# Kernel tuning notes

Measured on AMD Instinct MI355X. Metric: run time of the kernel, lower is better.

The kernel has to match this reference:

```python
import jax, jax.numpy as jnp
import numpy as np

N_NODES = 50000
N_EDGES = 800000
N_FEAT = 256


def setup_inputs() -> dict:
    key = jax.random.key(0)
    k_h, k_src, k_dst, k_w1, k_w2 = jax.random.split(key, 5)
    h = jax.random.normal(k_h, (N_NODES, N_FEAT), dtype=jnp.float32)
    src = jax.random.randint(k_src, (N_EDGES,), 0, N_NODES, dtype=jnp.int32)
    dst = jax.random.randint(k_dst, (N_EDGES,), 0, N_NODES, dtype=jnp.int32)
    # Kaiming-uniform-ish init like nn.Linear defaults
    b1 = 1.0 / np.sqrt(2 * N_FEAT)
    b2 = 1.0 / np.sqrt(N_FEAT)
    W1_w = jax.random.uniform(k_w1, (N_FEAT, 2 * N_FEAT), dtype=jnp.float32, minval=-b1, maxval=b1)
    W1_b = jnp.zeros((N_FEAT,), dtype=jnp.float32)
    W2_w = jax.random.uniform(k_w2, (1, N_FEAT), dtype=jnp.float32, minval=-b2, maxval=b2)
    W2_b = jnp.zeros((1,), dtype=jnp.float32)
    return {"h": h, "src": src, "dst": dst, "W1_w": W1_w, "W1_b": W1_b, "W2_w": W2_w, "W2_b": W2_b}


def reference(h, src, dst, W1_w, W1_b, W2_w, W2_b):
    # Gather per-edge endpoint features and concat along feature dim: [E, 2F]
    e = jnp.concatenate([h[src], h[dst]], axis=-1)
    # 2-layer MLP: Linear -> ReLU -> Linear, squeeze to per-edge score [E]
    hid = jax.nn.relu(e @ W1_w.T + W1_b)          # [E, F]
    score = (hid @ W2_w.T + W2_b)[:, 0]            # [E]
    return score
```

## Files before the change

### kernel.cpp

```cpp
#include <hip/hip_runtime.h>

#define F 256
#define TWO_F 512
#define BM 128
#define BN 64
#define BK 64
#define NBKT 512
#define EPB 4096

typedef __attribute__((ext_vector_type(8))) short short8;
typedef __attribute__((ext_vector_type(4))) float float4v;

static __device__ __forceinline__ unsigned short f2bf(float f) {
    unsigned u = __float_as_uint(f);
    u += 0x7FFFu + ((u >> 16) & 1u);
    return (unsigned short)(u >> 16);
}
static __device__ __forceinline__ unsigned pack2(float lo, float hi) {
    unsigned a = __float_as_uint(lo) + 0x8000u;
    unsigned b = __float_as_uint(hi) + 0x8000u;
    return __builtin_amdgcn_perm(b, a, 0x07060302u);
}
static __device__ __forceinline__ float blo(unsigned u) { return __uint_as_float(u << 16); }
static __device__ __forceinline__ float rawf(unsigned u) { return __uint_as_float(u); }

__global__ __launch_bounds__(256) void prep_kernel(
    const float* __restrict__ h, const float* __restrict__ W1,
    unsigned short* __restrict__ hb, unsigned short* __restrict__ Wb, int M)
{
    int i = blockIdx.x * blockDim.x + threadIdx.x;
    if (i < M * 128) {
        int m = i >> 7;
        int kp = (i & 127) * 2;
        float2 v = *(const float2*)(h + (size_t)m * F + kp);
        unsigned pk = pack2(v.x, v.y);
        int ksw = ((kp & 63) + (m & 7) * 8) & 63;
        *(unsigned*)(hb + (size_t)m * F + (kp & ~63) + ksw) = pk;
    }
    if (i < TWO_F * F) {
        int n = i >> 8;
        int k = i & 255;
        float v = W1[(n & 255) * TWO_F + ((n >> 8) << 8) + k];
        int kin_sw = ((k & 63) + (n & 7) * 8) & 63;
        Wb[n * F + (k & ~63) + kin_sw] = f2bf(v);
    }
}

__global__ __launch_bounds__(256, 3) void gemm_kernel(
    const unsigned short* __restrict__ hb, const unsigned short* __restrict__ Wb,
    const float* __restrict__ b1v, unsigned short* __restrict__ C, int M)
{
    __shared__ unsigned short sA[2][BM * BK];
    __shared__ unsigned short sB[2][BN * BK];

    const int ib = blockIdx.x;
    const int r8 = ib & 7;
    const int q  = ib >> 3;
    const int by = q & 7;
    const int bx = (q >> 3) * 8 + r8;
    const int bm = bx * BM;
    if (bm >= M) return;
    const int bn = by * BN;

    const int tid  = threadIdx.x;
    const int lane = tid & 63;
    const int wid  = tid >> 6;
    const int st_r = lane >> 3;
    const int st_k = (lane & 7) * 8;
    const int quad = lane >> 4;
    const int l15  = lane & 15;
    const int rot  = (l15 & 7) * 8;

    float4v acc[2][4];
    #pragma unroll
    for (int i = 0; i < 2; ++i)
        #pragma unroll
        for (int j = 0; j < 4; ++j) acc[i][j] = (float4v)(0.f);

    auto stage = [&](int buf, int k0) {
        #pragma unroll
        for (int p = 0; p < 4; ++p) {
            int r = wid * 32 + p * 8;
            int am = bm + r + st_r; if (am > M - 1) am = M - 1;
            const unsigned short* ga = hb + (size_t)am * F + k0 + st_k;
            __builtin_amdgcn_global_load_lds(
                (const __attribute__((address_space(1))) unsigned int*)ga,
                (__attribute__((address_space(3))) unsigned int*)&sA[buf][r * BK],
                16, 0, 0);
        }
        #pragma unroll
        for (int p = 0; p < 2; ++p) {
            int r = wid * 16 + p * 8;
            const unsigned short* gb = Wb + (size_t)(bn + r + st_r) * F + k0 + st_k;
            __builtin_amdgcn_global_load_lds(
                (const __attribute__((address_space(1))) unsigned int*)gb,
                (__attribute__((address_space(3))) unsigned int*)&sB[buf][r * BK],
                16, 0, 0);
        }
    };

    stage(0, 0);

    #pragma unroll
    for (int kt = 0; kt < 4; ++kt) {
        const int cur = kt & 1;
        __syncthreads();
        if (kt < 3) stage(cur ^ 1, (kt + 1) * BK);

        #pragma unroll
        for (int ks = 0; ks < 2; ++ks) {
            const int koff = (ks * 32 + quad * 8 + rot) & 63;
            short8 afr[2], bfr[4];
            #pragma unroll
            for (int mt = 0; mt < 2; ++mt)
                afr[mt] = *(const short8*)&sA[cur][(wid * 32 + mt * 16 + l15) * BK + koff];
            #pragma unroll
            for (int nt = 0; nt < 4; ++nt)
                bfr[nt] = *(const short8*)&sB[cur][(nt * 16 + l15) * BK + koff];
            #pragma unroll
            for (int mt = 0; mt < 2; ++mt)
                #pragma unroll
                for (int nt = 0; nt < 4; ++nt)
                    acc[mt][nt] = __builtin_amdgcn_mfma_f32_16x16x32_bf16(
                        afr[mt], bfr[nt], acc[mt][nt], 0, 0, 0);
        }
    }

    float bias[4];
    #pragma unroll
    for (int nt = 0; nt < 4; ++nt) {
        int n = bn + nt * 16 + l15;
        bias[nt] = (n < F) ? b1v[n] : 0.f;
    }
    #pragma unroll
    for (int mt = 0; mt < 2; ++mt) {
        #pragma unroll
        for (int rr = 0; rr < 4; ++rr) {
            int row = wid * 32 + mt * 16 + quad * 4 + rr;
            #pragma unroll
            for (int nt = 0; nt < 4; ++nt)
                sA[0][row * BK + nt * 16 + l15] = f2bf(acc[mt][nt][rr] + bias[nt]);
        }
    }
    __syncthreads();
    #pragma unroll
    for (int p = 0; p < 4; ++p) {
        int row = p * 32 + (tid >> 3);
        int gm = bm + row;
        if (gm < M) {
            uint4 v = *(const uint4*)&sA[0][row * BK + (tid & 7) * 8];
            *(uint4*)(C + (size_t)gm * TWO_F + bn + (tid & 7) * 8) = v;
        }
    }
}

__global__ __launch_bounds__(256) void sort_count_kernel(
    const int* __restrict__ src, int* __restrict__ counts, int E)
{
    __shared__ int cnt[NBKT];
    const int tid = threadIdx.x;
    #pragma unroll
    for (int i = tid; i < NBKT; i += 256) cnt[i] = 0;
    __syncthreads();
    const int base = blockIdx.x * EPB;
    #pragma unroll
    for (int j = 0; j < EPB / 256; ++j) {
        int e = base + j * 256 + tid;
        if (e < E) atomicAdd(&cnt[((unsigned)src[e]) >> 7], 1);
    }
    __syncthreads();
    #pragma unroll
    for (int i = tid; i < NBKT; i += 256) counts[blockIdx.x * NBKT + i] = cnt[i];
}

__global__ __launch_bounds__(512) void sort_scan_kernel(
    int* __restrict__ counts, int* __restrict__ bucketbase, int nsb)
{
    __shared__ int s[NBKT];
    const int tid = threadIdx.x;
    int run = 0;
    int blk = 0;
    for (; blk + 8 <= nsb; blk += 8) {
        int v[8];
        #pragma unroll
        for (int u = 0; u < 8; ++u) v[u] = counts[(blk + u) * NBKT + tid];
        #pragma unroll
        for (int u = 0; u < 8; ++u) { counts[(blk + u) * NBKT + tid] = run; run += v[u]; }
    }
    for (; blk < nsb; ++blk) {
        int v = counts[blk * NBKT + tid];
        counts[blk * NBKT + tid] = run;
        run += v;
    }
    s[tid] = run;
    __syncthreads();
    #pragma unroll
    for (int off = 1; off < NBKT; off <<= 1) {
        int x = (tid >= off) ? s[tid - off] : 0;
        __syncthreads();
        s[tid] += x;
        __syncthreads();
    }
    bucketbase[tid] = s[tid] - run;
}

__global__ __launch_bounds__(256) void sort_scatter_kernel(
    const int* __restrict__ src, const int* __restrict__ dst,
    const int* __restrict__ counts, const int* __restrict__ bucketbase,
    int2* __restrict__ sort_sd, int* __restrict__ sort_idx, int E)
{
    __shared__ int cnt[NBKT];
    const int tid = threadIdx.x;
    #pragma unroll
    for (int i = tid; i < NBKT; i += 256) cnt[i] = 0;
    __syncthreads();
    const int base = blockIdx.x * EPB;
    #pragma unroll
    for (int j = 0; j < EPB / 256; ++j) {
        int e = base + j * 256 + tid;
        if (e < E) {
            int s = src[e];
            int b = ((unsigned)s) >> 7;
            int r = atomicAdd(&cnt[b], 1);
            int pos = bucketbase[b] + counts[blockIdx.x * NBKT + b] + r;
            sort_sd[pos] = make_int2(s, dst[e]);
            sort_idx[pos] = e;
        }
    }
}

__global__ __launch_bounds__(256) void edge_kernel(
    const unsigned short* __restrict__ C,
    const int2* __restrict__ sd, const int* __restrict__ sidx,
    const float* __restrict__ w2,
    const float* __restrict__ b2, float* __restrict__ out, int E)
{
    const int lane = threadIdx.x & 31;
    const int nblk = gridDim.x;
    const int ib = blockIdx.x;
    const int gb = (nblk & 7) == 0 ? ((ib & 7) * (nblk >> 3) + (ib >> 3)) : ib;
    const int g = gb * 8 + (threadIdx.x >> 5);
    const int e0 = g * 2;
    if (e0 >= E) return;
    const bool has1 = (e0 + 1 < E);
    int2 p0 = sd[e0];
    int2 p1 = has1 ? sd[e0 + 1] : p0;
    int i0 = sidx[e0];
    int i1 = has1 ? sidx[e0 + 1] : 0;

    uint4 av0 = *(const uint4*)(C + (size_t)p0.x * TWO_F + lane * 8);
    uint4 bv0 = *(const uint4*)(C + (size_t)p0.y * TWO_F + F + lane * 8);
    uint4 av1 = *(const uint4*)(C + (size_t)p1.x * TWO_F + lane * 8);
    uint4 bv1 = *(const uint4*)(C + (size_t)p1.y * TWO_F + F + lane * 8);
    float4 w0 = *(const float4*)(w2 + lane * 8);
    float4 w1 = *(const float4*)(w2 + lane * 8 + 4);

    float sum0, sum1;
    sum0  = w0.x * fmaxf(blo(av0.x) + blo(bv0.x), 0.f);
    sum0 += w0.y * fmaxf(rawf(av0.x) + rawf(bv0.x), 0.f);
    sum0 += w0.z * fmaxf(blo(av0.y) + blo(bv0.y), 0.f);
    sum0 += w0.w * fmaxf(rawf(av0.y) + rawf(bv0.y), 0.f);
    sum0 += w1.x * fmaxf(blo(av0.z) + blo(bv0.z), 0.f);
    sum0 += w1.y * fmaxf(rawf(av0.z) + rawf(bv0.z), 0.f);
    sum0 += w1.z * fmaxf(blo(av0.w) + blo(bv0.w), 0.f);
    sum0 += w1.w * fmaxf(rawf(av0.w) + rawf(bv0.w), 0.f);

    sum1  = w0.x * fmaxf(blo(av1.x) + blo(bv1.x), 0.f);
    sum1 += w0.y * fmaxf(rawf(av1.x) + rawf(bv1.x), 0.f);
    sum1 += w0.z * fmaxf(blo(av1.y) + blo(bv1.y), 0.f);
    sum1 += w0.w * fmaxf(rawf(av1.y) + rawf(bv1.y), 0.f);
    sum1 += w1.x * fmaxf(blo(av1.z) + blo(bv1.z), 0.f);
    sum1 += w1.y * fmaxf(rawf(av1.z) + rawf(bv1.z), 0.f);
    sum1 += w1.z * fmaxf(blo(av1.w) + blo(bv1.w), 0.f);
    sum1 += w1.w * fmaxf(rawf(av1.w) + rawf(bv1.w), 0.f);

    #pragma unroll
    for (int off = 16; off > 0; off >>= 1) {
        sum0 += __shfl_down(sum0, off, 32);
        sum1 += __shfl_down(sum1, off, 32);
    }

    if (lane == 0) {
        float b = b2[0];
        out[i0] = sum0 + b;
        if (has1) out[i1] = sum1 + b;
    }
}

extern "C" void kernel_launch(void* const* d_in, const int* in_sizes, int n_in,
                              void* d_out, int out_size, void* d_ws, size_t ws_size,
                              hipStream_t stream) {
    const float* h    = (const float*)d_in[0];
    const int*   src  = (const int*)d_in[1];
    const int*   dst  = (const int*)d_in[2];
    const float* W1_w = (const float*)d_in[3];
    const float* W1_b = (const float*)d_in[4];
    const float* W2_w = (const float*)d_in[5];
    const float* W2_b = (const float*)d_in[6];
    float* out = (float*)d_out;

    const int M = in_sizes[0] / F;
    const int E = in_sizes[1];

    unsigned short* Wb = (unsigned short*)d_ws;
    unsigned short* hb = (unsigned short*)((char*)d_ws + 512 * 1024);
    unsigned short* C  = (unsigned short*)((char*)d_ws + 512 * 1024 + 26 * 1024 * 1024);
    int2* sort_sd    = (int2*)hb;
    int*  sort_idx   = (int*)((char*)hb + 8 * 1024 * 1024);
    int*  counts     = (int*)((char*)hb + 12 * 1024 * 1024);
    int*  bucketbase = (int*)((char*)hb + 13 * 1024 * 1024);

    int prep_threads = M * 128 > TWO_F * F ? M * 128 : TWO_F * F;
    prep_kernel<<<(prep_threads + 255) / 256, 256, 0, stream>>>(h, W1_w, hb, Wb, M);

    int nbx = ((M + BM - 1) / BM + 7) / 8 * 8;
    gemm_kernel<<<nbx * 8, 256, 0, stream>>>(hb, Wb, W1_b, C, M);

    int nsb = (E + EPB - 1) / EPB;
    sort_count_kernel<<<nsb, 256, 0, stream>>>(src, counts, E);
    sort_scan_kernel<<<1, 512, 0, stream>>>(counts, bucketbase, nsb);
    sort_scatter_kernel<<<nsb, 256, 0, stream>>>(src, dst, counts, bucketbase, sort_sd, sort_idx, E);

    int eblocks = (E / 2 + 7) / 8;
    edge_kernel<<<eblocks, 256, 0, stream>>>(C, sort_sd, sort_idx, W2_w, W2_b, out, E);
}
```

Measured before the change: 243.2 us.

## Load A fragments directly from global, stage full W tile in LDS once

The GEMM kernel no longer double-buffers A and B tiles through LDS. It stages the whole 64x256 weight slice into shared memory once and reads the swizzled bf16 activation rows directly from global memory into MFMA fragments. This removes the per-k-step barriers and the LDS traffic for A, and raises occupancy to 4 waves per SIMD. In exchange, A reads become per-lane 16-byte global loads that are not coalesced across rows, with no overlap pipelining. Separately, the edges-per-block count in the sort kernels is doubled.

Measured after the change: 244.4 us. About the same (+0.5%).

```diff
diff --git a/kernel.cpp b/kernel.cpp
--- a/kernel.cpp
+++ b/kernel.cpp
@@ -6,7 +6,7 @@
 #define BN 64
 #define BK 64
 #define NBKT 512
-#define EPB 4096
+#define EPB 8192
 
 typedef __attribute__((ext_vector_type(8))) short short8;
 typedef __attribute__((ext_vector_type(4))) float float4v;
@@ -46,12 +46,11 @@
     }
 }
 
-__global__ __launch_bounds__(256, 3) void gemm_kernel(
+__global__ __launch_bounds__(256, 4) void gemm_kernel(
     const unsigned short* __restrict__ hb, const unsigned short* __restrict__ Wb,
     const float* __restrict__ b1v, unsigned short* __restrict__ C, int M)
 {
-    __shared__ unsigned short sA[2][BM * BK];
-    __shared__ unsigned short sB[2][BN * BK];
+    __shared__ unsigned short sB[BN * F];
 
     const int ib = blockIdx.x;
     const int r8 = ib & 7;
@@ -65,58 +64,47 @@
     const int tid  = threadIdx.x;
     const int lane = tid & 63;
     const int wid  = tid >> 6;
-    const int st_r = lane >> 3;
-    const int st_k = (lane & 7) * 8;
     const int quad = lane >> 4;
     const int l15  = lane & 15;
     const int rot  = (l15 & 7) * 8;
 
+    #pragma unroll
+    for (int p = 0; p < 8; ++p) {
+        const unsigned short* gb = Wb + (size_t)(bn + p * 8 + (tid >> 5)) * F + (tid & 31) * 8;
+        __builtin_amdgcn_global_load_lds(
+            (const __attribute__((address_space(1))) unsigned int*)gb,
+            (__attribute__((address_space(3))) unsigned int*)&sB[p * 2048 + tid * 8],
+            16, 0, 0);
+    }
+
+    const unsigned short* arow[2];
+    #pragma unroll
+    for (int mt = 0; mt < 2; ++mt) {
+        int am = bm + wid * 32 + mt * 16 + l15;
+        if (am > M - 1) am = M - 1;
+        arow[mt] = hb + (size_t)am * F;
+    }
+
     float4v acc[2][4];
     #pragma unroll
     for (int i = 0; i < 2; ++i)
         #pragma unroll
         for (int j = 0; j < 4; ++j) acc[i][j] = (float4v)(0.f);
 
-    auto stage = [&](int buf, int k0) {
-        #pragma unroll
-        for (int p = 0; p < 4; ++p) {
-            int r = wid * 32 + p * 8;
-            int am = bm + r + st_r; if (am > M - 1) am = M - 1;
-            const unsigned short* ga = hb + (size_t)am * F + k0 + st_k;
-            __builtin_amdgcn_global_load_lds(
-                (const __attribute__((address_space(1))) unsigned int*)ga,
-                (__attribute__((address_space(3))) unsigned int*)&sA[buf][r * BK],
-                16, 0, 0);
-        }
-        #pragma unroll
-        for (int p = 0; p < 2; ++p) {
-            int r = wid * 16 + p * 8;
-            const unsigned short* gb = Wb + (size_t)(bn + r + st_r) * F + k0 + st_k;
-            __builtin_amdgcn_global_load_lds(
-                (const __attribute__((address_space(1))) unsigned int*)gb,
-                (__attribute__((address_space(3))) unsigned int*)&sB[buf][r * BK],
-                16, 0, 0);
-        }
-    };
-
-    stage(0, 0);
+    __syncthreads();
 
     #pragma unroll
     for (int kt = 0; kt < 4; ++kt) {
-        const int cur = kt & 1;
-        __syncthreads();
-        if (kt < 3) stage(cur ^ 1, (kt + 1) * BK);
-
         #pragma unroll
         for (int ks = 0; ks < 2; ++ks) {
-            const int koff = (ks * 32 + quad * 8 + rot) & 63;
+            const int koff = kt * 64 + ((ks * 32 + quad * 8 + rot) & 63);
             short8 afr[2], bfr[4];
             #pragma unroll
             for (int mt = 0; mt < 2; ++mt)
-                afr[mt] = *(const short8*)&sA[cur][(wid * 32 + mt * 16 + l15) * BK + koff];
+                afr[mt] = *(const short8*)(arow[mt] + koff);
             #pragma unroll
             for (int nt = 0; nt < 4; ++nt)
-                bfr[nt] = *(const short8*)&sB[cur][(nt * 16 + l15) * BK + koff];
+                bfr[nt] = *(const short8*)&sB[(nt * 16 + l15) * F + koff];
             #pragma unroll
             for (int mt = 0; mt < 2; ++mt)
                 #pragma unroll
@@ -132,6 +120,7 @@
         int n = bn + nt * 16 + l15;
         bias[nt] = (n < F) ? b1v[n] : 0.f;
     }
+    __syncthreads();
     #pragma unroll
     for (int mt = 0; mt < 2; ++mt) {
         #pragma unroll
@@ -139,7 +128,7 @@
             int row = wid * 32 + mt * 16 + quad * 4 + rr;
             #pragma unroll
             for (int nt = 0; nt < 4; ++nt)
-                sA[0][row * BK + nt * 16 + l15] = f2bf(acc[mt][nt][rr] + bias[nt]);
+                sB[row * BK + nt * 16 + l15] = f2bf(acc[mt][nt][rr] + bias[nt]);
         }
     }
     __syncthreads();
@@ -148,7 +137,7 @@
         int row = p * 32 + (tid >> 3);
         int gm = bm + row;
         if (gm < M) {
-            uint4 v = *(const uint4*)&sA[0][row * BK + (tid & 7) * 8];
+            uint4 v = *(const uint4*)&sB[row * BK + (tid & 7) * 8];
             *(uint4*)(C + (size_t)gm * TWO_F + bn + (tid & 7) * 8) = v;
         }
     }
```
